# Optimization experiments

Hardware: AMD Instinct MI355X
Metric: run time of the kernel (lower is better)

Reference implementation:

```python
import jax, jax.numpy as jnp
import numpy as np

L, B, D = 1024, 24, 512


def setup_inputs() -> dict:
    key = jax.random.key(0)
    ks = jax.random.split(key, 9)
    s = 1.0 / np.sqrt(D)
    return {
        "v": jax.random.normal(ks[0], (L, B, D), dtype=jnp.float32),
        "h0": jax.random.normal(ks[1], (B, D), dtype=jnp.float32),
        "V": jax.random.normal(ks[2], (B, D), dtype=jnp.float32),
        "Wp": jax.random.normal(ks[3], (D, D), dtype=jnp.float32) * s,
        "Wp_": jax.random.normal(ks[4], (D, D), dtype=jnp.float32) * s,
        "w_ih": jax.random.normal(ks[5], (3 * D, D), dtype=jnp.float32) * s,
        "w_hh": jax.random.normal(ks[6], (3 * D, D), dtype=jnp.float32) * s,
        "b_ih": jax.random.normal(ks[7], (3 * D,), dtype=jnp.float32) * s,
        "b_hh": jax.random.normal(ks[8], (3 * D,), dtype=jnp.float32) * s,
    }


def reference(v, h0, V, Wp, Wp_, w_ih, w_hh, b_ih, b_hh):
    # v: [l, b, d]. Precompute both projections once (original wastefully
    # recomputes Wp_(v) per step; the math is identical).
    Wpv_all = jnp.einsum('lbd,hd->lbh', v, Wp)    # per-step query proj
    Wpvp = jnp.einsum('lbd,hd->lbh', v, Wp_)      # shared key proj

    def step(h, wpv_i):
        # additive attention over all l positions
        x = jnp.tanh(wpv_i[None, :, :] + Wpvp)           # [l, b, h]
        s = jnp.einsum('lbh,bh->bl', x, V)               # scores
        a = jax.nn.softmax(s, axis=1)                    # [b, l]
        c = jnp.einsum('bl,lbd->bd', a, v)               # context [b, d]
        # torch.nn.GRUCell math
        gi = c @ w_ih.T + b_ih
        gh = h @ w_hh.T + b_hh
        i_r, i_z, i_n = jnp.split(gi, 3, axis=1)
        h_r, h_z, h_n = jnp.split(gh, 3, axis=1)
        r = jax.nn.sigmoid(i_r + h_r)
        z = jax.nn.sigmoid(i_z + h_z)
        n = jnp.tanh(i_n + r * h_n)
        h_new = (1.0 - z) * n + z * h
        return h_new, h_new

    _, hs = jax.lax.scan(step, h0, Wpv_all)              # hs: [l, b, d]
    # dropout is identity in eval mode
    return hs
```

## Files before the change

### kernel.cpp

```cpp
#include <hip/hip_runtime.h>
#include <math.h>


__launch_bounds__(256, 2)
__global__ void gemm_abt_kernel(const float* __restrict__ A, const float* __restrict__ B,
                                float* __restrict__ out, int K, int N,
                                const float* __restrict__ bias, int do_tanh) {
  __shared__ __align__(16) float As[16][136];
  __shared__ __align__(16) float Bs[16][136];
  const int m0 = blockIdx.y * 128, n0 = blockIdx.x * 128;
  const int tid = threadIdx.x;
  const int tm = (tid & 15) * 8, tn = (tid >> 4) * 8;
  const int srow = tid & 127, scol = (tid >> 7) * 8;
  const float* Ap = A + (size_t)(m0 + srow) * K + scol;
  const float* Bp = B + (size_t)(n0 + srow) * K + scol;
  float acc[8][8] = {{0.f}};
  for (int k0 = 0; k0 < K; k0 += 16) {
    const float4 a0 = *(const float4*)(Ap + k0);
    const float4 a1 = *(const float4*)(Ap + k0 + 4);
    const float4 b0 = *(const float4*)(Bp + k0);
    const float4 b1 = *(const float4*)(Bp + k0 + 4);
    __syncthreads();
    As[scol + 0][srow] = a0.x; As[scol + 1][srow] = a0.y;
    As[scol + 2][srow] = a0.z; As[scol + 3][srow] = a0.w;
    As[scol + 4][srow] = a1.x; As[scol + 5][srow] = a1.y;
    As[scol + 6][srow] = a1.z; As[scol + 7][srow] = a1.w;
    Bs[scol + 0][srow] = b0.x; Bs[scol + 1][srow] = b0.y;
    Bs[scol + 2][srow] = b0.z; Bs[scol + 3][srow] = b0.w;
    Bs[scol + 4][srow] = b1.x; Bs[scol + 5][srow] = b1.y;
    Bs[scol + 6][srow] = b1.z; Bs[scol + 7][srow] = b1.w;
    __syncthreads();
#pragma unroll
    for (int kk = 0; kk < 16; ++kk) {
      const float4 av0 = *(const float4*)&As[kk][tm];
      const float4 av1 = *(const float4*)&As[kk][tm + 4];
      const float4 bv0 = *(const float4*)&Bs[kk][tn];
      const float4 bv1 = *(const float4*)&Bs[kk][tn + 4];
      const float ar[8] = {av0.x, av0.y, av0.z, av0.w, av1.x, av1.y, av1.z, av1.w};
      const float br[8] = {bv0.x, bv0.y, bv0.z, bv0.w, bv1.x, bv1.y, bv1.z, bv1.w};
#pragma unroll
      for (int r = 0; r < 8; ++r)
#pragma unroll
        for (int c = 0; c < 8; ++c)
          acc[r][c] = fmaf(ar[r], br[c], acc[r][c]);
    }
  }
#pragma unroll
  for (int r = 0; r < 8; ++r) {
    float* o = out + (size_t)(m0 + tm + r) * N + n0 + tn;
#pragma unroll
    for (int c = 0; c < 8; ++c) {
      float val = acc[r][c];
      if (bias) val += bias[n0 + tn + c];
      if (do_tanh) val = tanhf(val);
      o[c] = val;
    }
  }
}

__launch_bounds__(256, 3)
__global__ void attn_kernel(const float* __restrict__ tq, const float* __restrict__ tk,
                            const float* __restrict__ Vv, const float* __restrict__ v,
                            float* __restrict__ Cout) {
  const int b = blockIdx.y;
  const int it = blockIdx.x;
  const int tid = threadIdx.x;
  const int wave = tid >> 6, lane = tid & 63;
  const int h8 = lane * 8;
  __shared__ __align__(16) float sm[4][1024];
  __shared__ __align__(16) float red[4][4][512];
  __shared__ float inv_s[4];

  float q[4][8], vp[4][8];
  {
    const float* vvp = Vv + (size_t)b * 512 + h8;
    const float4 v0 = *(const float4*)vvp;
    const float4 v1 = *(const float4*)(vvp + 4);
    const float vv[8] = {v0.x, v0.y, v0.z, v0.w, v1.x, v1.y, v1.z, v1.w};
#pragma unroll
    for (int ii = 0; ii < 4; ++ii) {
      const float* qp = tq + ((size_t)(it * 4 + ii) * 24 + b) * 512 + h8;
      const float4 q0 = *(const float4*)qp;
      const float4 q1 = *(const float4*)(qp + 4);
      q[ii][0] = q0.x; q[ii][1] = q0.y; q[ii][2] = q0.z; q[ii][3] = q0.w;
      q[ii][4] = q1.x; q[ii][5] = q1.y; q[ii][6] = q1.z; q[ii][7] = q1.w;
#pragma unroll
      for (int j = 0; j < 8; ++j)
        vp[ii][j] = vv[j] * (1.0f - q[ii][j] * q[ii][j]);
    }
  }

  for (int l = wave; l < 1024; l += 4) {
    const float* kp = tk + ((size_t)l * 24 + b) * 512 + h8;
    const float4 k0 = *(const float4*)kp;
    const float4 k1 = *(const float4*)(kp + 4);
    const float kkv[8] = {k0.x, k0.y, k0.z, k0.w, k1.x, k1.y, k1.z, k1.w};
    float acc0 = 0.f, acc1 = 0.f, acc2 = 0.f, acc3 = 0.f;
#pragma unroll
    for (int j = 0; j < 8; ++j) {
      const float w = kkv[j];
      acc0 = fmaf(vp[0][j] * w, __builtin_amdgcn_rcpf(fmaf(q[0][j], w, 1.0f)), acc0);
      acc1 = fmaf(vp[1][j] * w, __builtin_amdgcn_rcpf(fmaf(q[1][j], w, 1.0f)), acc1);
      acc2 = fmaf(vp[2][j] * w, __builtin_amdgcn_rcpf(fmaf(q[2][j], w, 1.0f)), acc2);
      acc3 = fmaf(vp[3][j] * w, __builtin_amdgcn_rcpf(fmaf(q[3][j], w, 1.0f)), acc3);
    }
#pragma unroll
    for (int mask = 32; mask; mask >>= 1) {
      acc0 += __shfl_xor(acc0, mask, 64);
      acc1 += __shfl_xor(acc1, mask, 64);
      acc2 += __shfl_xor(acc2, mask, 64);
      acc3 += __shfl_xor(acc3, mask, 64);
    }
    if (lane == 0) {
      sm[0][l] = acc0; sm[1][l] = acc1; sm[2][l] = acc2; sm[3][l] = acc3;
    }
  }
  __syncthreads();

  {
    float* row = sm[wave];
    float m = -1e30f;
    for (int t = lane; t < 1024; t += 64) m = fmaxf(m, row[t]);
#pragma unroll
    for (int mask = 32; mask; mask >>= 1) m = fmaxf(m, __shfl_xor(m, mask, 64));
    float s = 0.f;
    for (int t = lane; t < 1024; t += 64) {
      const float e = __expf(row[t] - m);
      row[t] = e;
      s += e;
    }
#pragma unroll
    for (int mask = 32; mask; mask >>= 1) s += __shfl_xor(s, mask, 64);
    if (lane == 0) inv_s[wave] = 1.0f / s;
  }
  __syncthreads();

  float ca[4][8] = {{0.f}};
  const int l0 = wave * 256;
  for (int l = l0; l < l0 + 256; ++l) {
    const float* vrow = v + ((size_t)l * 24 + b) * 512 + h8;
    const float4 x0 = *(const float4*)vrow;
    const float4 x1 = *(const float4*)(vrow + 4);
    const float a0 = sm[0][l], a1 = sm[1][l], a2 = sm[2][l], a3 = sm[3][l];
    const float xv[8] = {x0.x, x0.y, x0.z, x0.w, x1.x, x1.y, x1.z, x1.w};
#pragma unroll
    for (int j = 0; j < 8; ++j) {
      ca[0][j] = fmaf(a0, xv[j], ca[0][j]);
      ca[1][j] = fmaf(a1, xv[j], ca[1][j]);
      ca[2][j] = fmaf(a2, xv[j], ca[2][j]);
      ca[3][j] = fmaf(a3, xv[j], ca[3][j]);
    }
  }
#pragma unroll
  for (int ii = 0; ii < 4; ++ii) {
    *(float4*)&red[wave][ii][h8]     = make_float4(ca[ii][0], ca[ii][1], ca[ii][2], ca[ii][3]);
    *(float4*)&red[wave][ii][h8 + 4] = make_float4(ca[ii][4], ca[ii][5], ca[ii][6], ca[ii][7]);
  }
  __syncthreads();
  {
    const int ii = tid >> 6;
    const int d0 = (tid & 63) * 8;
    float4 s0 = *(const float4*)&red[0][ii][d0];
    float4 s1 = *(const float4*)&red[0][ii][d0 + 4];
#pragma unroll
    for (int w = 1; w < 4; ++w) {
      const float4 r0 = *(const float4*)&red[w][ii][d0];
      const float4 r1 = *(const float4*)&red[w][ii][d0 + 4];
      s0.x += r0.x; s0.y += r0.y; s0.z += r0.z; s0.w += r0.w;
      s1.x += r1.x; s1.y += r1.y; s1.z += r1.z; s1.w += r1.w;
    }
    const float inv = inv_s[ii];
    s0.x *= inv; s0.y *= inv; s0.z *= inv; s0.w *= inv;
    s1.x *= inv; s1.y *= inv; s1.z *= inv; s1.w *= inv;
    float* o = Cout + ((size_t)(it * 4 + ii) * 24 + b) * 512 + d0;
    *(float4*)o = s0;
    *(float4*)(o + 4) = s1;
  }
}

union HPack {
  unsigned long long u;
  struct { float f; unsigned tag; } s;
};

__launch_bounds__(512, 1)
__global__ void gru_persist_kernel(const float* __restrict__ Gi_c,
                                   const float* __restrict__ w_hh,
                                   const float* __restrict__ b_hh,
                                   const float* __restrict__ h0,
                                   unsigned long long* __restrict__ hb0,
                                   unsigned long long* __restrict__ hb1,
                                   float* __restrict__ out, int gstep0) {
  const int g  = blockIdx.x & 7;
  const int sl = blockIdx.x >> 3;
  const int t = threadIdx.x;
  const int d_loc = t & 63;
  const int kc = t >> 6;
  const int dglob = sl * 64 + d_loc;

  __shared__ __align__(16) float h_lds[512];
  __shared__ float red[3][64][9];

  float wreg[3][64];
#pragma unroll
  for (int gg = 0; gg < 3; ++gg) {
    const float* wr = w_hh + (size_t)(gg * 512 + dglob) * 512 + kc * 64;
#pragma unroll
    for (int j = 0; j < 64; j += 4) {
      const float4 wv = *(const float4*)(wr + j);
      wreg[gg][j] = wv.x; wreg[gg][j + 1] = wv.y; wreg[gg][j + 2] = wv.z; wreg[gg][j + 3] = wv.w;
    }
  }
  const float bias_r = b_hh[dglob];
  const float bias_z = b_hh[512 + dglob];
  const float bias_n = b_hh[1024 + dglob];

  if (gstep0 == 0 && t < 192) {
    const int q = t >> 6, d = t & 63;
    const int bg = g * 3 + q;
    HPack p;
    p.s.f = h0[(size_t)bg * 512 + sl * 64 + d];
    p.s.tag = 1u;
    __hip_atomic_store(hb1 + (size_t)bg * 512 + sl * 64 + d, p.u,
                       __ATOMIC_RELAXED, __HIP_MEMORY_SCOPE_AGENT);
  }

  float hq[3];
  HPack pf;
  pf.u = __hip_atomic_load(((gstep0 & 1) ? hb0 : hb1) + (size_t)(g * 3) * 512 + t,
                           __ATOMIC_RELAXED, __HIP_MEMORY_SCOPE_AGENT);

  for (int il = 0; il < 128; ++il) {
    const int gs = gstep0 + il;
#pragma unroll
    for (int q = 0; q < 3; ++q) {
      const int bg = g * 3 + q;
      const unsigned want = (unsigned)(gs + 1);
      const unsigned long long* src = ((gs & 1) ? hb0 : hb1) + (size_t)bg * 512 + t;

      HPack p = pf;
      {
        const int gs_n = (q == 2) ? gs + 1 : gs;
        const int bg_n = (q == 2) ? g * 3 : bg + 1;
        pf.u = __hip_atomic_load(((gs_n & 1) ? hb0 : hb1) + (size_t)bg_n * 512 + t,
                                 __ATOMIC_RELAXED, __HIP_MEMORY_SCOPE_AGENT);
      }
      while (p.s.tag < want) {
        __builtin_amdgcn_s_sleep(1);
        p.u = __hip_atomic_load(src, __ATOMIC_RELAXED, __HIP_MEMORY_SCOPE_AGENT);
      }
      h_lds[t] = p.s.f;

      float gir = 0.f, giz = 0.f, gin = 0.f;
      if (t < 64) {
        const float* gi = Gi_c + ((size_t)il * 24 + bg) * 1536;
        gir = gi[dglob]; giz = gi[512 + dglob]; gin = gi[1024 + dglob];
      }
      __syncthreads();
      if (il == 0 && t < 64) hq[q] = h_lds[dglob];

      float a0 = 0.f, a1 = 0.f, a2 = 0.f, b0 = 0.f, b1 = 0.f, b2 = 0.f;
#pragma unroll
      for (int j = 0; j < 64; j += 8) {
        const float4 h1 = *(const float4*)&h_lds[kc * 64 + j];
        const float4 h2 = *(const float4*)&h_lds[kc * 64 + j + 4];
        a0 = fmaf(h1.x, wreg[0][j], fmaf(h1.y, wreg[0][j+1], fmaf(h1.z, wreg[0][j+2], fmaf(h1.w, wreg[0][j+3], a0))));
        b0 = fmaf(h2.x, wreg[0][j+4], fmaf(h2.y, wreg[0][j+5], fmaf(h2.z, wreg[0][j+6], fmaf(h2.w, wreg[0][j+7], b0))));
        a1 = fmaf(h1.x, wreg[1][j], fmaf(h1.y, wreg[1][j+1], fmaf(h1.z, wreg[1][j+2], fmaf(h1.w, wreg[1][j+3], a1))));
        b1 = fmaf(h2.x, wreg[1][j+4], fmaf(h2.y, wreg[1][j+5], fmaf(h2.z, wreg[1][j+6], fmaf(h2.w, wreg[1][j+7], b1))));
        a2 = fmaf(h1.x, wreg[2][j], fmaf(h1.y, wreg[2][j+1], fmaf(h1.z, wreg[2][j+2], fmaf(h1.w, wreg[2][j+3], a2))));
        b2 = fmaf(h2.x, wreg[2][j+4], fmaf(h2.y, wreg[2][j+5], fmaf(h2.z, wreg[2][j+6], fmaf(h2.w, wreg[2][j+7], b2))));
      }
      red[0][d_loc][kc] = a0 + b0;
      red[1][d_loc][kc] = a1 + b1;
      red[2][d_loc][kc] = a2 + b2;
      __syncthreads();

      if (t < 64) {
        const float* r0 = red[0][t];
        const float* r1 = red[1][t];
        const float* r2 = red[2][t];
        const float sr = ((r0[0] + r0[1]) + (r0[2] + r0[3])) + ((r0[4] + r0[5]) + (r0[6] + r0[7]));
        const float sz = ((r1[0] + r1[1]) + (r1[2] + r1[3])) + ((r1[4] + r1[5]) + (r1[6] + r1[7]));
        const float sn = ((r2[0] + r2[1]) + (r2[2] + r2[3])) + ((r2[4] + r2[5]) + (r2[6] + r2[7]));
        const float r = __builtin_amdgcn_rcpf(1.0f + __expf(-(gir + sr + bias_r)));
        const float z = __builtin_amdgcn_rcpf(1.0f + __expf(-(giz + sz + bias_z)));
        const float nx = gin + r * (sn + bias_n);
        const float e2 = __expf(-2.0f * fabsf(nx));
        const float tn = __builtin_copysignf((1.0f - e2) * __builtin_amdgcn_rcpf(1.0f + e2), nx);
        const float hn = (1.0f - z) * tn + z * hq[q];
        hq[q] = hn;
        HPack pw; pw.s.f = hn; pw.s.tag = (unsigned)(gs + 2);
        __hip_atomic_store(((gs & 1) ? hb1 : hb0) + (size_t)bg * 512 + dglob, pw.u,
                           __ATOMIC_RELAXED, __HIP_MEMORY_SCOPE_AGENT);
        out[((size_t)gs * 24 + bg) * 512 + dglob] = hn;
      }
    }
  }
}

extern "C" void kernel_launch(void* const* d_in, const int* in_sizes, int n_in,
                              void* d_out, int out_size, void* d_ws, size_t ws_size,
                              hipStream_t stream) {
  (void)in_sizes; (void)n_in; (void)out_size;
  const float* v    = (const float*)d_in[0];
  const float* h0   = (const float*)d_in[1];
  const float* Vv   = (const float*)d_in[2];
  const float* Wp   = (const float*)d_in[3];
  const float* Wp_  = (const float*)d_in[4];
  const float* w_ih = (const float*)d_in[5];
  const float* w_hh = (const float*)d_in[6];
  const float* b_ih = (const float*)d_in[7];
  const float* b_hh = (const float*)d_in[8];
  float* out = (float*)d_out;

  const bool full_tq = ws_size >= (size_t)126025728;
  float* ws   = (float*)d_ws;
  float* tk   = ws;
  float* tqF  = tk + (size_t)12582912;
  float* tq_c = tk + (size_t)12582912;
  float* C_c  = full_tq ? (tqF + (size_t)12582912) : (tq_c + (size_t)1572864);
  float* Gi_c = C_c + (size_t)1572864;
  unsigned long long* hb0 = (unsigned long long*)(Gi_c + (size_t)4718592);
  unsigned long long* hb1 = hb0 + (size_t)12288;

  hipMemsetAsync(hb0, 0, (size_t)2 * 12288 * sizeof(unsigned long long), stream);

  gemm_abt_kernel<<<dim3(4, 192), 256, 0, stream>>>(v, Wp_, tk, 512, 512, nullptr, 1);
  if (full_tq)
    gemm_abt_kernel<<<dim3(4, 192), 256, 0, stream>>>(v, Wp, tqF, 512, 512, nullptr, 1);

  for (int c = 0; c < 8; ++c) {
    const float* v_chunk = v + (size_t)c * 128 * 24 * 512;
    const float* tq_use;
    if (full_tq) {
      tq_use = tqF + (size_t)c * 128 * 24 * 512;
    } else {
      gemm_abt_kernel<<<dim3(4, 24), 256, 0, stream>>>(v_chunk, Wp, tq_c, 512, 512, nullptr, 1);
      tq_use = tq_c;
    }
    attn_kernel<<<dim3(32, 24), 256, 0, stream>>>(tq_use, tk, Vv, v, C_c);
    gemm_abt_kernel<<<dim3(12, 24), 256, 0, stream>>>(C_c, w_ih, Gi_c, 512, 1536, b_ih, 0);
    gru_persist_kernel<<<64, 512, 0, stream>>>(Gi_c, w_hh, b_hh, h0, hb0, hb1,
                                               out, c * 128);
  }
}
```

Measured before the change: 8.118 ms.

## Replace LDS reduction with wavefront shuffles and double-buffer hidden-state LDS

Remaps threads so the eight k-chunks of one output sit in adjacent lanes of a wavefront, which lets the partial dot products be reduced with xor shuffles instead of an LDS array and a second block barrier. The h buffer is double-buffered, with per-chunk padding to avoid bank conflicts, so one __syncthreads per sub-step is enough. The Gi loads are hoisted ahead of the spin-wait. This shortens the serial per-step critical path of the recurrent kernel, at the cost of spreading the gate math over 64 lanes across 8 wavefronts.

```diff
diff --git a/kernel.cpp b/kernel.cpp
--- a/kernel.cpp
+++ b/kernel.cpp
@@ -194,12 +194,15 @@
   const int g  = blockIdx.x & 7;
   const int sl = blockIdx.x >> 3;
   const int t = threadIdx.x;
-  const int d_loc = t & 63;
-  const int kc = t >> 6;
-  const int dglob = sl * 64 + d_loc;
-
-  __shared__ __align__(16) float h_lds[512];
-  __shared__ float red[3][64][9];
+  const int w = t >> 6;
+  const int l = t & 63;
+  const int og = l >> 3;
+  const int kc = l & 7;
+  const int d_w = w * 8 + og;
+  const int dglob = sl * 64 + d_w;
+  const bool pub = (kc == 0);
+
+  __shared__ __align__(16) float h_lds[2][544];
 
   float wreg[3][64];
 #pragma unroll
@@ -245,25 +248,26 @@
         pf.u = __hip_atomic_load(((gs_n & 1) ? hb0 : hb1) + (size_t)bg_n * 512 + t,
                                  __ATOMIC_RELAXED, __HIP_MEMORY_SCOPE_AGENT);
       }
+      float gir = 0.f, giz = 0.f, gin = 0.f;
+      if (pub) {
+        const float* gi = Gi_c + ((size_t)il * 24 + bg) * 1536 + dglob;
+        gir = gi[0]; giz = gi[512]; gin = gi[1024];
+      }
       while (p.s.tag < want) {
         __builtin_amdgcn_s_sleep(1);
         p.u = __hip_atomic_load(src, __ATOMIC_RELAXED, __HIP_MEMORY_SCOPE_AGENT);
       }
-      h_lds[t] = p.s.f;
-
-      float gir = 0.f, giz = 0.f, gin = 0.f;
-      if (t < 64) {
-        const float* gi = Gi_c + ((size_t)il * 24 + bg) * 1536;
-        gir = gi[dglob]; giz = gi[512 + dglob]; gin = gi[1024 + dglob];
-      }
+      const int buf = (il + q) & 1;
+      h_lds[buf][t + ((t >> 6) << 2)] = p.s.f;
       __syncthreads();
-      if (il == 0 && t < 64) hq[q] = h_lds[dglob];
-
+      if (il == 0 && pub) hq[q] = h_lds[buf][dglob + ((dglob >> 6) << 2)];
+
+      const float* hbp = &h_lds[buf][kc * 68];
       float a0 = 0.f, a1 = 0.f, a2 = 0.f, b0 = 0.f, b1 = 0.f, b2 = 0.f;
 #pragma unroll
       for (int j = 0; j < 64; j += 8) {
-        const float4 h1 = *(const float4*)&h_lds[kc * 64 + j];
-        const float4 h2 = *(const float4*)&h_lds[kc * 64 + j + 4];
+        const float4 h1 = *(const float4*)(hbp + j);
+        const float4 h2 = *(const float4*)(hbp + j + 4);
         a0 = fmaf(h1.x, wreg[0][j], fmaf(h1.y, wreg[0][j+1], fmaf(h1.z, wreg[0][j+2], fmaf(h1.w, wreg[0][j+3], a0))));
         b0 = fmaf(h2.x, wreg[0][j+4], fmaf(h2.y, wreg[0][j+5], fmaf(h2.z, wreg[0][j+6], fmaf(h2.w, wreg[0][j+7], b0))));
         a1 = fmaf(h1.x, wreg[1][j], fmaf(h1.y, wreg[1][j+1], fmaf(h1.z, wreg[1][j+2], fmaf(h1.w, wreg[1][j+3], a1))));
@@ -271,18 +275,15 @@
         a2 = fmaf(h1.x, wreg[2][j], fmaf(h1.y, wreg[2][j+1], fmaf(h1.z, wreg[2][j+2], fmaf(h1.w, wreg[2][j+3], a2))));
         b2 = fmaf(h2.x, wreg[2][j+4], fmaf(h2.y, wreg[2][j+5], fmaf(h2.z, wreg[2][j+6], fmaf(h2.w, wreg[2][j+7], b2))));
       }
-      red[0][d_loc][kc] = a0 + b0;
-      red[1][d_loc][kc] = a1 + b1;
-      red[2][d_loc][kc] = a2 + b2;
-      __syncthreads();
-
-      if (t < 64) {
-        const float* r0 = red[0][t];
-        const float* r1 = red[1][t];
-        const float* r2 = red[2][t];
-        const float sr = ((r0[0] + r0[1]) + (r0[2] + r0[3])) + ((r0[4] + r0[5]) + (r0[6] + r0[7]));
-        const float sz = ((r1[0] + r1[1]) + (r1[2] + r1[3])) + ((r1[4] + r1[5]) + (r1[6] + r1[7]));
-        const float sn = ((r2[0] + r2[1]) + (r2[2] + r2[3])) + ((r2[4] + r2[5]) + (r2[6] + r2[7]));
+      float sr = a0 + b0, sz = a1 + b1, sn = a2 + b2;
+#pragma unroll
+      for (int mask = 1; mask <= 4; mask <<= 1) {
+        sr += __shfl_xor(sr, mask, 64);
+        sz += __shfl_xor(sz, mask, 64);
+        sn += __shfl_xor(sn, mask, 64);
+      }
+
+      if (pub) {
         const float r = __builtin_amdgcn_rcpf(1.0f + __expf(-(gir + sr + bias_r)));
         const float z = __builtin_amdgcn_rcpf(1.0f + __expf(-(giz + sz + bias_z)));
         const float nx = gin + r * (sn + bias_n);
```

Measured after the change: 8.414 ms. +3.6%, slower.
